# Kernel optimization log

Hardware: AMD Instinct MI355X
Metric: run time of the kernel (lower is better)

Reference implementation:

```python
import jax, jax.numpy as jnp
import numpy as np

N = 30000
E = 300000
F_IN = 512
OUT = 1024


def _l2norm(x):
    # F.normalize(x, p=2, dim=1) with eps=1e-12
    n = jnp.linalg.norm(x, axis=1, keepdims=True)
    return x / jnp.maximum(n, 1e-12)


def _gcn_conv(x, W, b, row, col, w):
    # PyG GCNConv: x' = D^-1/2 (A + I) D^-1/2 (x W) + b, self-loops weight 1
    n = x.shape[0]
    h = x @ W  # [n, out]
    deg = jax.ops.segment_sum(w, row, num_segments=n)
    dinv = jnp.where(deg > 0, jax.lax.rsqrt(deg), 0.0)
    nw = dinv[row] * w * dinv[col]  # per-edge norm
    agg = jax.ops.segment_sum(h[col] * nw[:, None], row, num_segments=n)
    return agg + b


def _forward(x, edge_index, edge_weight, beta,
             W1, b1, W2, b2, W3, b3, Wmu, bmu, Wlv, blv, Wd1, bd1, Wd2, bd2):
    n = x.shape[0]
    loops = jnp.arange(n, dtype=edge_index.dtype)
    row = jnp.concatenate([edge_index[0], loops])
    col = jnp.concatenate([edge_index[1], loops])
    w = jnp.concatenate([edge_weight, jnp.ones((n,), edge_weight.dtype)])

    out1 = jax.nn.relu(_l2norm(_gcn_conv(x, W1, b1, row, col, w)))
    out2 = jax.nn.relu(_l2norm(_gcn_conv(out1, W2, b2, row, col, w)))
    out3 = jax.nn.relu(_l2norm(_gcn_conv(out2, W3, b3, row, col, w)))

    mu = out3 @ Wmu + bmu
    logvar = out3 @ Wlv + blv

    # reparameterize(mu, beta * logvar) with eps ~ N(0,1)*0.01
    lv = beta * logvar
    std = jnp.exp(0.5 * lv)
    eps = jax.random.normal(jax.random.key(42), std.shape, std.dtype) * 0.01
    z = mu + eps * std

    # batch=None pooling: global max + mean over nodes
    pooled = jnp.concatenate([jnp.max(z, axis=0), jnp.mean(z, axis=0)])[None, :]  # [1, 1024]

    h = jax.nn.relu(pooled @ Wd1 + bd1)
    recon_x = jax.nn.sigmoid(h @ Wd2 + bd2)
    return recon_x, mu, logvar


def setup_inputs() -> dict:
    key = jax.random.key(0)
    ks = jax.random.split(key, 20)
    def glorot(k, shape):
        lim = np.sqrt(6.0 / (shape[0] + shape[1]))
        return jax.random.uniform(k, shape, jnp.float32, -lim, lim)
    H = 512
    return {
        "x": jax.random.normal(ks[0], (N, F_IN), jnp.float32),
        "edge_index": jax.random.randint(ks[1], (2, E), 0, N, jnp.int64),
        "edge_weight": jax.random.uniform(ks[2], (E,), jnp.float32),
        "beta": 1,
        "W1": glorot(ks[3], (F_IN, 1024)), "b1": jnp.zeros((1024,), jnp.float32),
        "W2": glorot(ks[4], (1024, 512)), "b2": jnp.zeros((512,), jnp.float32),
        "W3": glorot(ks[5], (512, 256)), "b3": jnp.zeros((256,), jnp.float32),
        "Wmu": glorot(ks[6], (256, H)), "bmu": jnp.zeros((H,), jnp.float32),
        "Wlv": glorot(ks[7], (256, H)), "blv": jnp.zeros((H,), jnp.float32),
        "Wd1": glorot(ks[8], (2 * H, 2 * H)), "bd1": jnp.zeros((2 * H,), jnp.float32),
        "Wd2": glorot(ks[9], (2 * H, OUT)), "bd2": jnp.zeros((OUT,), jnp.float32),
    }


def reference(x, edge_index, edge_weight, beta,
              W1, b1, W2, b2, W3, b3, Wmu, bmu, Wlv, blv, Wd1, bd1, Wd2, bd2):
    return _forward(x, edge_index, edge_weight, beta,
                    W1, b1, W2, b2, W3, b3, Wmu, bmu, Wlv, blv, Wd1, bd1, Wd2, bd2)
```

## Files before the change

kernel.cpp:

```cpp
#include <hip/hip_runtime.h>
#include <cstdint>
#include <cstddef>

#define NNODE      30000
#define FIN        512
#define H1DIM      1024
#define H2DIM      512
#define H3DIM      256
#define HDIM       512
#define HALF_ROWS  15000
#define HALF_ELEMS 7680000u
#define PP_ROWS    16
#define PP_BLOCKS  938
#define PM_BLOCKS  64
#define NPANEL     118
#define NSCAN      118

typedef __attribute__((ext_vector_type(8))) short s16x8;
typedef __attribute__((ext_vector_type(4))) short s16x4;
typedef __attribute__((ext_vector_type(4))) float f32x4;

__device__ __forceinline__ short f2bf(float f) {
    uint32_t u = __float_as_uint(f);
    uint32_t r = (u + 0x7FFFu + ((u >> 16) & 1u)) >> 16;
    return (short)r;
}
__device__ __forceinline__ float bf2f(short s) {
    return __uint_as_float(((uint32_t)(uint16_t)s) << 16);
}

__device__ __forceinline__ void threefry2x32(uint32_t k0, uint32_t k1,
                                             uint32_t& x0, uint32_t& x1) {
    uint32_t ks0 = k0, ks1 = k1, ks2 = k0 ^ k1 ^ 0x1BD11BDAu;
    const uint32_t R0[4] = {13u, 15u, 26u, 6u};
    const uint32_t R1[4] = {17u, 29u, 16u, 24u};
    x0 += ks0; x1 += ks1;
#pragma unroll
    for (int g = 0; g < 5; ++g) {
        const uint32_t* R = (g & 1) ? R1 : R0;
#pragma unroll
        for (int r = 0; r < 4; ++r) {
            x0 += x1;
            x1 = (x1 << R[r]) | (x1 >> (32u - R[r]));
            x1 ^= x0;
        }
        uint32_t ks_a = (g % 3 == 0) ? ks1 : (g % 3 == 1 ? ks2 : ks0);
        uint32_t ks_b = (g % 3 == 0) ? ks2 : (g % 3 == 1 ? ks0 : ks1);
        x0 += ks_a;
        x1 += ks_b + (uint32_t)(g + 1);
    }
}

__device__ __forceinline__ float jax_normal(uint32_t bits) {
    uint32_t fb = (bits >> 9) | 0x3F800000u;
    float f = __uint_as_float(fb) - 1.0f;
    const float lo = -0.99999994f;
    float u = fmaf(f, 2.0f, lo);
    u = fmaxf(u, lo);
    return 1.41421356237f * erfinvf(u);
}

__global__ void deg_cnt_kernel(const int* __restrict__ row, const float* __restrict__ w,
                               float* __restrict__ deg, int* __restrict__ cnt, int E) {
    int e = blockIdx.x * 256 + threadIdx.x;
    if (e < E) {
        int r = row[e];
        atomicAdd(&deg[r], w[e]);
        atomicAdd(&cnt[r], 1);
    }
}

__global__ void dinv_kernel(const float* __restrict__ deg, float* __restrict__ dinv, int n) {
    int i = blockIdx.x * 256 + threadIdx.x;
    if (i < n) dinv[i] = rsqrtf(deg[i] + 1.0f);
}

__global__ void rsqrt_clamp_kernel(float* __restrict__ ss, int n) {
    int i = blockIdx.x * 256 + threadIdx.x;
    if (i < n) ss[i] = 1.0f / fmaxf(sqrtf(ss[i]), 1e-12f);
}

__global__ __launch_bounds__(256) void rp_blocksum(const int* __restrict__ cnt,
                                                   int* __restrict__ bsum) {
    __shared__ int sh[256];
    int i = blockIdx.x * 256 + threadIdx.x;
    sh[threadIdx.x] = (i < NNODE) ? cnt[i] : 0;
    __syncthreads();
    for (int o = 128; o; o >>= 1) {
        if (threadIdx.x < o) sh[threadIdx.x] += sh[threadIdx.x + o];
        __syncthreads();
    }
    if (threadIdx.x == 0) bsum[blockIdx.x] = sh[0];
}

__global__ __launch_bounds__(128) void rp_scan(int* __restrict__ bsum, int nb) {
    __shared__ int sh[128];
    int t = threadIdx.x;
    sh[t] = (t < nb) ? bsum[t] : 0;
    __syncthreads();
    for (int o = 1; o < 128; o <<= 1) {
        int v = (t >= o) ? sh[t - o] : 0;
        __syncthreads();
        sh[t] += v;
        __syncthreads();
    }
    if (t < nb) bsum[t] = (t == 0) ? 0 : sh[t - 1];
}

__global__ __launch_bounds__(256) void rp_write(const int* __restrict__ cnt,
                                                const int* __restrict__ bsum,
                                                int* __restrict__ rowptr, int E) {
    __shared__ int sh[256];
    int i = blockIdx.x * 256 + threadIdx.x;
    int v = (i < NNODE) ? cnt[i] : 0;
    sh[threadIdx.x] = v;
    __syncthreads();
    for (int o = 1; o < 256; o <<= 1) {
        int x = (threadIdx.x >= o) ? sh[threadIdx.x - o] : 0;
        __syncthreads();
        sh[threadIdx.x] += x;
        __syncthreads();
    }
    if (i < NNODE) rowptr[i] = bsum[blockIdx.x] + sh[threadIdx.x] - v;
    if (i == NNODE - 1) rowptr[NNODE] = E;
}

__global__ void scatter_edges(const int* __restrict__ row, const int* __restrict__ col,
                              const float* __restrict__ w, const float* __restrict__ dinv,
                              const int* __restrict__ rowptr, int* __restrict__ fill,
                              int* __restrict__ ecol, float* __restrict__ eval, int E) {
    int e = blockIdx.x * 256 + threadIdx.x;
    if (e < E) {
        int r = row[e], c = col[e];
        int pos = rowptr[r] + atomicAdd(&fill[r], 1);
        ecol[pos] = c;
        eval[pos] = dinv[r] * w[e] * dinv[c];
    }
}

__global__ void f32_to_bf16(const float* __restrict__ in, short* __restrict__ out, int n4) {
    int i = blockIdx.x * 256 + threadIdx.x;
    if (i < n4) {
        float4 v = ((const float4*)in)[i];
        s16x4 s = { f2bf(v.x), f2bf(v.y), f2bf(v.z), f2bf(v.w) };
        *(s16x4*)(out + (size_t)i * 4) = s;
    }
}

__global__ __launch_bounds__(256) void transpose_bf16(const float* __restrict__ W,
                                                      short* __restrict__ Wt, int K, int N) {
    __shared__ float t[32][33];
    int kb = blockIdx.y * 32, nb = blockIdx.x * 32;
    int tx = threadIdx.x & 31, ty = threadIdx.x >> 5;
#pragma unroll
    for (int i = 0; i < 32; i += 8)
        if (kb + ty + i < K && nb + tx < N)
            t[ty + i][tx] = W[(size_t)(kb + ty + i) * N + nb + tx];
    __syncthreads();
#pragma unroll
    for (int i = 0; i < 32; i += 8)
        if (nb + ty + i < N && kb + tx < K)
            Wt[(size_t)(nb + ty + i) * K + kb + tx] = f2bf(t[tx][ty + i]);
}

template <int F, bool FUSE>
__global__ __launch_bounds__(256) void spmm_bf16(const int* __restrict__ rowptr,
                                                 const int* __restrict__ ecol,
                                                 const float* __restrict__ eval,
                                                 const float* __restrict__ dinv,
                                                 const short* __restrict__ h,
                                                 const float* __restrict__ bias,
                                                 short* __restrict__ out) {
    constexpr int NE = F / 64;
    int lane = threadIdx.x & 63;
    int r = blockIdx.x * 4 + (threadIdx.x >> 6);
    if (r >= NNODE) return;
    float d = dinv[r];
    float dd = d * d;
    float acc[NE];
    {
        const short* p = h + (size_t)r * F + lane * NE;
        if constexpr (NE == 8) {
            s16x8 v = *(const s16x8*)p;
#pragma unroll
            for (int j = 0; j < 8; ++j) acc[j] = dd * bf2f(v[j]);
        } else {
            s16x4 v = *(const s16x4*)p;
#pragma unroll
            for (int j = 0; j < 4; ++j) acc[j] = dd * bf2f(v[j]);
        }
    }
    int e0 = rowptr[r], e1 = rowptr[r + 1];
    int e = e0;
    for (; e + 2 <= e1; e += 2) {
        int c0 = ecol[e], c1 = ecol[e + 1];
        float w0 = eval[e], w1 = eval[e + 1];
        const short* p0 = h + (size_t)c0 * F + lane * NE;
        const short* p1 = h + (size_t)c1 * F + lane * NE;
        if constexpr (NE == 8) {
            s16x8 v0 = *(const s16x8*)p0;
            s16x8 v1 = *(const s16x8*)p1;
#pragma unroll
            for (int j = 0; j < 8; ++j) acc[j] = fmaf(w0, bf2f(v0[j]), acc[j]);
#pragma unroll
            for (int j = 0; j < 8; ++j) acc[j] = fmaf(w1, bf2f(v1[j]), acc[j]);
        } else {
            s16x4 v0 = *(const s16x4*)p0;
            s16x4 v1 = *(const s16x4*)p1;
#pragma unroll
            for (int j = 0; j < 4; ++j) acc[j] = fmaf(w0, bf2f(v0[j]), acc[j]);
#pragma unroll
            for (int j = 0; j < 4; ++j) acc[j] = fmaf(w1, bf2f(v1[j]), acc[j]);
        }
    }
    if (e < e1) {
        int c = ecol[e];
        float nw = eval[e];
        const short* p = h + (size_t)c * F + lane * NE;
        if constexpr (NE == 8) {
            s16x8 v = *(const s16x8*)p;
#pragma unroll
            for (int j = 0; j < 8; ++j) acc[j] = fmaf(nw, bf2f(v[j]), acc[j]);
        } else {
            s16x4 v = *(const s16x4*)p;
#pragma unroll
            for (int j = 0; j < 4; ++j) acc[j] = fmaf(nw, bf2f(v[j]), acc[j]);
        }
    }
    short* o = out + (size_t)r * F + lane * NE;
    if (FUSE) {
        const float* bp = bias + lane * NE;
        float ss = 0.f;
#pragma unroll
        for (int j = 0; j < NE; ++j) { acc[j] += bp[j]; ss += acc[j] * acc[j]; }
#pragma unroll
        for (int off = 32; off; off >>= 1) ss += __shfl_xor(ss, off);
        float rinv = 1.0f / fmaxf(sqrtf(ss), 1e-12f);
#pragma unroll
        for (int j = 0; j < NE; ++j) acc[j] = fmaxf(acc[j] * rinv, 0.f);
    }
    if constexpr (NE == 8) {
        s16x8 s;
#pragma unroll
        for (int j = 0; j < 8; ++j) s[j] = f2bf(acc[j]);
        *(s16x8*)o = s;
    } else {
        s16x4 s;
#pragma unroll
        for (int j = 0; j < 4; ++j) s[j] = f2bf(acc[j]);
        *(s16x4*)o = s;
    }
}

#define STAGE_TILE(buf_, kt_)                                                              \
  {                                                                                        \
    const int k0_ = (kt_) << 6;                                                            \
    _Pragma("unroll")                                                                      \
    for (int i_ = 0; i_ < 4; ++i_) {                                                       \
      int c_ = i_ * 8 + w;                                                                 \
      int tr_ = c_ * 8 + srow;                                                             \
      __builtin_amdgcn_global_load_lds(                                                    \
          (const __attribute__((address_space(1))) void*)(A + (size_t)(m0 + tr_) * K + k0_ + scol), \
          (__attribute__((address_space(3))) void*)(&sA[buf_][c_ * 512]), 16, 0, 0);       \
    }                                                                                      \
    _Pragma("unroll")                                                                      \
    for (int i_ = 0; i_ < 4; ++i_) {                                                       \
      int c_ = i_ * 8 + w;                                                                 \
      int tr_ = c_ * 8 + srow;                                                             \
      __builtin_amdgcn_global_load_lds(                                                    \
          (const __attribute__((address_space(1))) void*)(Bt + (size_t)(n0 + tr_) * K + k0_ + scol), \
          (__attribute__((address_space(3))) void*)(&sB[buf_][c_ * 512]), 16, 0, 0);       \
    }                                                                                      \
  }

template <typename OutT, bool ADD_BIAS, int EPI>
__global__ __launch_bounds__(512) void gemm_bf16(const short* __restrict__ A,
                                                 const short* __restrict__ Bt,
                                                 const float* __restrict__ bias,
                                                 const float* __restrict__ bias2,
                                                 OutT* __restrict__ C,
                                                 float* __restrict__ C2,
                                                 float* __restrict__ ssbuf,
                                                 int M, int N, int K) {
    __shared__ short sA[2][256 * 64];
    __shared__ short sB[2][256 * 64];
    const int tid = threadIdx.x;
    const int lane = tid & 63;
    const int w = tid >> 6;
    const int wm = w >> 2, wn = w & 3;

    const int nwg = gridDim.x;
    const int orig = blockIdx.x;
    const int q = nwg >> 3, rr = nwg & 7;
    const int xcd = orig & 7;
    const int base = (xcd < rr) ? xcd * (q + 1) : rr * (q + 1) + (xcd - rr) * q;
    const int wgid = base + (orig >> 3);
    const int nx = N >> 8;
    const int lg = __builtin_ctz(nx);
    const int pid = wgid >> lg;
    const int cblk = wgid & (nx - 1);
    const int m0 = pid << 8;
    const int n0 = cblk << 8;

    const int srow = lane >> 3;
    const int scol = ((lane & 7) ^ srow) * 8;

    f32x4 acc[8][4] = {};

    const int lrow = lane & 15;
    const int jhi = lane >> 4;

    const int nkt = K >> 6;
    int cur = 0;
    STAGE_TILE(0, 0);
    __syncthreads();

    for (int kt = 0; kt < nkt; ++kt) {
        if (kt + 1 < nkt) STAGE_TILE(cur ^ 1, kt + 1);

        s16x8 bfr[4][2];
#pragma unroll
        for (int fn = 0; fn < 4; ++fn) {
            int lr = wn * 64 + fn * 16 + lrow;
            const short* bptr = &sB[cur][lr * 64];
            int sl0 = jhi ^ (lr & 7);
            bfr[fn][0] = *(const s16x8*)&bptr[sl0 << 3];
            bfr[fn][1] = *(const s16x8*)&bptr[(sl0 ^ 4) << 3];
        }
        __builtin_amdgcn_s_setprio(1);
#pragma unroll
        for (int fm = 0; fm < 8; ++fm) {
            int lr = wm * 128 + fm * 16 + lrow;
            const short* aptr = &sA[cur][lr * 64];
            int sl0 = jhi ^ (lr & 7);
            s16x8 a0 = *(const s16x8*)&aptr[sl0 << 3];
            s16x8 a1 = *(const s16x8*)&aptr[(sl0 ^ 4) << 3];
#pragma unroll
            for (int fn = 0; fn < 4; ++fn) {
                acc[fm][fn] = __builtin_amdgcn_mfma_f32_16x16x32_bf16(a0, bfr[fn][0], acc[fm][fn], 0, 0, 0);
                acc[fm][fn] = __builtin_amdgcn_mfma_f32_16x16x32_bf16(a1, bfr[fn][1], acc[fm][fn], 0, 0, 0);
            }
        }
        __builtin_amdgcn_s_setprio(0);
        __syncthreads();
        cur ^= 1;
    }

    const int crow = (lane >> 4) * 4;
    const int ccol = lane & 15;

    if constexpr (EPI == 1) {
        float ssl[8][4] = {};
#pragma unroll
        for (int fm = 0; fm < 8; ++fm) {
#pragma unroll
            for (int fn = 0; fn < 4; ++fn) {
                int n = n0 + wn * 64 + fn * 16 + ccol;
                float b = bias[n];
#pragma unroll
                for (int r = 0; r < 4; ++r) {
                    float o = acc[fm][fn][r] + b;
                    ssl[fm][r] += o * o;
                    int m = m0 + wm * 128 + fm * 16 + crow + r;
                    if (m < M) C[(size_t)m * N + n] = (OutT)f2bf(fmaxf(o, 0.f));
                }
            }
        }
#pragma unroll
        for (int fm = 0; fm < 8; ++fm)
#pragma unroll
            for (int r = 0; r < 4; ++r) {
                float v = ssl[fm][r];
                v += __shfl_xor(v, 1); v += __shfl_xor(v, 2);
                v += __shfl_xor(v, 4); v += __shfl_xor(v, 8);
                int m = m0 + wm * 128 + fm * 16 + crow + r;
                if (ccol == 0 && m < M) atomicAdd(&ssbuf[m], v);
            }
    } else if constexpr (EPI == 2) {
#pragma unroll
        for (int fm = 0; fm < 8; ++fm) {
#pragma unroll
            for (int fn = 0; fn < 4; ++fn) {
                int n = n0 + wn * 64 + fn * 16 + ccol;
#pragma unroll
                for (int r = 0; r < 4; ++r) {
                    int m = m0 + wm * 128 + fm * 16 + crow + r;
                    if (m < M) {
                        float sc = ssbuf[m];
                        C[(size_t)m * N + n] = (OutT)f2bf(acc[fm][fn][r] * sc);
                    }
                }
            }
        }
    } else if constexpr (EPI == 3) {
        const int half = N >> 1;
#pragma unroll
        for (int fm = 0; fm < 8; ++fm) {
#pragma unroll
            for (int fn = 0; fn < 4; ++fn) {
                int n = n0 + wn * 64 + fn * 16 + ccol;
                bool hi = n >= half;
                float b = hi ? bias2[n - half] : bias[n];
                float* Cp = hi ? C2 : (float*)C;
                int nc = hi ? (n - half) : n;
#pragma unroll
                for (int r = 0; r < 4; ++r) {
                    int m = m0 + wm * 128 + fm * 16 + crow + r;
                    if (m < M) Cp[(size_t)m * half + nc] = acc[fm][fn][r] + b;
                }
            }
        }
    } else {
#pragma unroll
        for (int fm = 0; fm < 8; ++fm) {
#pragma unroll
            for (int fn = 0; fn < 4; ++fn) {
                int n = n0 + wn * 64 + fn * 16 + ccol;
                float b = ADD_BIAS ? bias[n] : 0.f;
#pragma unroll
                for (int r = 0; r < 4; ++r) {
                    int m = m0 + wm * 128 + fm * 16 + crow + r;
                    if (m < M) {
                        float o = acc[fm][fn][r] + b;
                        if constexpr (sizeof(OutT) == 2) C[(size_t)m * N + n] = (OutT)f2bf(o);
                        else                             C[(size_t)m * N + n] = o;
                    }
                }
            }
        }
    }
}

__global__ __launch_bounds__(256) void pool_partial(const float* __restrict__ mu,
                                                    const float* __restrict__ lv,
                                                    const uint32_t* __restrict__ beta_p,
                                                    float* __restrict__ pmax,
                                                    float* __restrict__ psum) {
    uint32_t bb = beta_p[0];
    float beta = (bb & 0x7F800000u) ? __uint_as_float(bb) : (float)(int)bb;
    int b = blockIdx.x;
    int r0 = b * PP_ROWS;
    int r1 = min(r0 + PP_ROWS, HALF_ROWS);
    int c = threadIdx.x * 2;
    float m0 = -INFINITY, m1 = -INFINITY, s0 = 0.f, s1 = 0.f;
    for (int r = r0; r < r1; ++r) {
        size_t ia = (size_t)r * HDIM + c;
        size_t ib = (size_t)(r + HALF_ROWS) * HDIM + c;
        float2 mua = *(const float2*)&mu[ia];
        float2 lva = *(const float2*)&lv[ia];
        float2 mub = *(const float2*)&mu[ib];
        float2 lvb = *(const float2*)&lv[ib];
        uint32_t idx0 = (uint32_t)r * 512u + (uint32_t)c;
        uint32_t xa0 = idx0,     ya0 = idx0 + HALF_ELEMS;
        uint32_t xa1 = idx0 + 1, ya1 = idx0 + 1 + HALF_ELEMS;
        threefry2x32(0u, 42u, xa0, ya0);
        threefry2x32(0u, 42u, xa1, ya1);
        float za0 = mua.x + 0.01f * jax_normal(xa0) * __expf(0.5f * beta * lva.x);
        float zb0 = mub.x + 0.01f * jax_normal(ya0) * __expf(0.5f * beta * lvb.x);
        float za1 = mua.y + 0.01f * jax_normal(xa1) * __expf(0.5f * beta * lva.y);
        float zb1 = mub.y + 0.01f * jax_normal(ya1) * __expf(0.5f * beta * lvb.y);
        m0 = fmaxf(m0, fmaxf(za0, zb0)); s0 += za0 + zb0;
        m1 = fmaxf(m1, fmaxf(za1, zb1)); s1 += za1 + zb1;
    }
    pmax[(size_t)b * HDIM + c]     = m0;
    pmax[(size_t)b * HDIM + c + 1] = m1;
    psum[(size_t)b * HDIM + c]     = s0;
    psum[(size_t)b * HDIM + c + 1] = s1;
}

__global__ __launch_bounds__(256) void pool_mid(const float* __restrict__ pmax,
                                                const float* __restrict__ psum,
                                                float* __restrict__ pmax2,
                                                float* __restrict__ psum2) {
    int g = blockIdx.x;
    int b0 = g * 15;
    int b1 = min(b0 + 15, PP_BLOCKS);
#pragma unroll
    for (int pass = 0; pass < 2; ++pass) {
        int c = threadIdx.x + pass * 256;
        float m = -INFINITY, s = 0.f;
        for (int b = b0; b < b1; ++b) {
            m = fmaxf(m, pmax[(size_t)b * HDIM + c]);
            s += psum[(size_t)b * HDIM + c];
        }
        pmax2[(size_t)g * HDIM + c] = m;
        psum2[(size_t)g * HDIM + c] = s;
    }
}

__global__ void pool_final(const float* __restrict__ pmax2, const float* __restrict__ psum2,
                           float* __restrict__ pooled) {
    int c = blockIdx.x * 256 + threadIdx.x;
    if (c < HDIM) {
        float m = -INFINITY, s = 0.f;
#pragma unroll
        for (int b = 0; b < PM_BLOCKS; ++b) {
            m = fmaxf(m, pmax2[(size_t)b * HDIM + c]);
            s += psum2[(size_t)b * HDIM + c];
        }
        pooled[c] = m;
        pooled[HDIM + c] = s / 30000.0f;
    }
}

__global__ __launch_bounds__(256) void dense_partial(const float* __restrict__ in,
                                                     const float* __restrict__ W,
                                                     float* __restrict__ part) {
    int by = blockIdx.y;
    int j = blockIdx.x * 256 + threadIdx.x;
    __shared__ float sin_[128];
    if (threadIdx.x < 128) sin_[threadIdx.x] = in[by * 128 + threadIdx.x];
    __syncthreads();
    float acc = 0.f;
#pragma unroll 8
    for (int i = 0; i < 128; ++i)
        acc = fmaf(sin_[i], W[(size_t)(by * 128 + i) * 1024 + j], acc);
    part[(size_t)by * 1024 + j] = acc;
}

__global__ void dense_final(const float* __restrict__ part, const float* __restrict__ bias,
                            float* __restrict__ out, int act) {
    int j = blockIdx.x * 256 + threadIdx.x;
    float acc = bias[j];
#pragma unroll
    for (int s = 0; s < 8; ++s) acc += part[(size_t)s * 1024 + j];
    out[j] = act ? (1.0f / (1.0f + __expf(-acc))) : fmaxf(acc, 0.f);
}

extern "C" void kernel_launch(void* const* d_in, const int* in_sizes, int n_in,
                              void* d_out, int out_size, void* d_ws, size_t ws_size,
                              hipStream_t stream) {
    const float* x   = (const float*)d_in[0];
    const int*   ei  = (const int*)d_in[1];
    const float* ew  = (const float*)d_in[2];
    const uint32_t* beta = (const uint32_t*)d_in[3];
    const float* W1  = (const float*)d_in[4];
    const float* b1  = (const float*)d_in[5];
    const float* W2  = (const float*)d_in[6];
    const float* b2  = (const float*)d_in[7];
    const float* W3  = (const float*)d_in[8];
    const float* b3  = (const float*)d_in[9];
    const float* Wmu = (const float*)d_in[10];
    const float* bmu = (const float*)d_in[11];
    const float* Wlv = (const float*)d_in[12];
    const float* blv = (const float*)d_in[13];
    const float* Wd1 = (const float*)d_in[14];
    const float* bd1 = (const float*)d_in[15];
    const float* Wd2 = (const float*)d_in[16];
    const float* bd2 = (const float*)d_in[17];

    const int E = in_sizes[2];
    const int M = NNODE;

    float* out    = (float*)d_out;
    float* mu_out = out + 1024;
    float* lv_out = out + 1024 + (size_t)M * HDIM;

    char* Wp = (char*)d_ws;
    short* slotA  = (short*)(Wp);
    short* slotB  = (short*)(Wp + 61603840);
    short* xb     = (short*)(Wp + 123207680);
    short* W1t    = (short*)(Wp + 154009600);
    short* W2t    = (short*)(Wp + 155058176);
    short* W3t    = (short*)(Wp + 156106752);
    short* Wmut   = (short*)(Wp + 156368896);
    short* Wlvt   = (short*)(Wp + 156631040);
    float* deg    = (float*)(Wp + 156893184);
    float* dinv   = (float*)(Wp + 157013184);
    int*   cnt    = (int*)  (Wp + 157133184);
    int*   fill   = (int*)  (Wp + 157253184);
    float* ssbuf  = (float*)(Wp + 157373184);
    int*   rowptr = (int*)  (Wp + 157493184);
    int*   ecol   = (int*)  (Wp + 157613188);
    float* eval   = (float*)(Wp + 158813188);
    float* pmax   = (float*)(Wp + 160013188);
    float* psum   = (float*)(Wp + 161934212);
    float* pmax2  = (float*)(Wp + 163855236);
    float* psum2  = (float*)(Wp + 163986308);
    float* pooled = (float*)(Wp + 164117380);
    float* hdec   = (float*)(Wp + 164121476);
    float* dpart  = (float*)(Wp + 164125572);
    int*   bsum   = (int*)pmax;

    const int* row = ei;
    const int* col = ei + E;

    hipMemsetAsync(deg, 0, 600000, stream);

    deg_cnt_kernel<<<(E + 255) / 256, 256, 0, stream>>>(row, ew, deg, cnt, E);
    dinv_kernel<<<(M + 255) / 256, 256, 0, stream>>>(deg, dinv, M);
    rp_blocksum<<<NSCAN, 256, 0, stream>>>(cnt, bsum);
    rp_scan<<<1, 128, 0, stream>>>(bsum, NSCAN);
    rp_write<<<NSCAN, 256, 0, stream>>>(cnt, bsum, rowptr, E);
    scatter_edges<<<(E + 255) / 256, 256, 0, stream>>>(row, col, ew, dinv, rowptr, fill,
                                                       ecol, eval, E);

    f32_to_bf16<<<(M * FIN / 4 + 255) / 256, 256, 0, stream>>>(x, xb, M * FIN / 4);
    {
        dim3 b(256);
        transpose_bf16<<<dim3(H1DIM / 32, FIN / 32),   b, 0, stream>>>(W1,  W1t,  FIN,   H1DIM);
        transpose_bf16<<<dim3(H2DIM / 32, H1DIM / 32), b, 0, stream>>>(W2,  W2t,  H1DIM, H2DIM);
        transpose_bf16<<<dim3(H3DIM / 32, H2DIM / 32), b, 0, stream>>>(W3,  W3t,  H2DIM, H3DIM);
        transpose_bf16<<<dim3(HDIM / 32,  H3DIM / 32), b, 0, stream>>>(Wmu, Wmut, H3DIM, HDIM);
        transpose_bf16<<<dim3(HDIM / 32,  H3DIM / 32), b, 0, stream>>>(Wlv, Wlvt, H3DIM, HDIM);
    }

    const int SPMM_GRID = (M + 3) / 4;

    spmm_bf16<512, false><<<SPMM_GRID, 256, 0, stream>>>(rowptr, ecol, eval, dinv, xb,
                                                         nullptr, slotA);
    gemm_bf16<short, true, 1><<<(H1DIM / 256) * NPANEL, 512, 0, stream>>>(
        slotA, W1t, b1, nullptr, slotB, nullptr, ssbuf, M, H1DIM, FIN);
    rsqrt_clamp_kernel<<<(M + 255) / 256, 256, 0, stream>>>(ssbuf, M);

    gemm_bf16<short, false, 2><<<(H2DIM / 256) * NPANEL, 512, 0, stream>>>(
        slotB, W2t, nullptr, nullptr, slotA, nullptr, ssbuf, M, H2DIM, H1DIM);
    spmm_bf16<512, true><<<SPMM_GRID, 256, 0, stream>>>(rowptr, ecol, eval, dinv, slotA,
                                                        b2, slotB);

    gemm_bf16<short, false, 0><<<(H3DIM / 256) * NPANEL, 512, 0, stream>>>(
        slotB, W3t, nullptr, nullptr, slotA, nullptr, nullptr, M, H3DIM, H2DIM);
    spmm_bf16<256, true><<<SPMM_GRID, 256, 0, stream>>>(rowptr, ecol, eval, dinv, slotA,
                                                        b3, slotB);

    gemm_bf16<float, true, 3><<<((2 * HDIM) / 256) * NPANEL, 512, 0, stream>>>(
        slotB, Wmut, bmu, blv, mu_out, lv_out, nullptr, M, 2 * HDIM, H3DIM);

    pool_partial<<<PP_BLOCKS, 256, 0, stream>>>(mu_out, lv_out, beta, pmax, psum);
    pool_mid<<<PM_BLOCKS, 256, 0, stream>>>(pmax, psum, pmax2, psum2);
    pool_final<<<2, 256, 0, stream>>>(pmax2, psum2, pooled);

    dense_partial<<<dim3(4, 8), 256, 0, stream>>>(pooled, Wd1, dpart);
    dense_final<<<4, 256, 0, stream>>>(dpart, bd1, hdec, 0);
    dense_partial<<<dim3(4, 8), 256, 0, stream>>>(hdec, Wd2, dpart);
    dense_final<<<4, 256, 0, stream>>>(dpart, bd2, out, 1);
}
```

Baseline: 492.1 us.

## Fold norm rsqrt into GEMM epilogue, unroll SpMM edges by four, finer pooling

Removes the standalone rsqrt_clamp kernel and computes the inverse L2 norm inside the EPI==2 GEMM epilogue, once per row instead of once per element load. The SpMM edge loop is unrolled from two to four neighbours to put more gathers in flight. Pool partial blocks are halved in rows and doubled in count, with the workspace offsets and the mid-level reduction resized to match. Each wave now repeats the sqrt/divide and carries more registers in the SpMM loop.

```diff
diff --git a/kernel.cpp b/kernel.cpp
--- a/kernel.cpp
+++ b/kernel.cpp
@@ -10,9 +10,9 @@
 #define HDIM       512
 #define HALF_ROWS  15000
 #define HALF_ELEMS 7680000u
-#define PP_ROWS    16
-#define PP_BLOCKS  938
-#define PM_BLOCKS  64
+#define PP_ROWS    8
+#define PP_BLOCKS  1875
+#define PM_BLOCKS  63
 #define NPANEL     118
 #define NSCAN      118
 
@@ -73,11 +73,6 @@
 __global__ void dinv_kernel(const float* __restrict__ deg, float* __restrict__ dinv, int n) {
     int i = blockIdx.x * 256 + threadIdx.x;
     if (i < n) dinv[i] = rsqrtf(deg[i] + 1.0f);
-}
-
-__global__ void rsqrt_clamp_kernel(float* __restrict__ ss, int n) {
-    int i = blockIdx.x * 256 + threadIdx.x;
-    if (i < n) ss[i] = 1.0f / fmaxf(sqrtf(ss[i]), 1e-12f);
 }
 
 __global__ __launch_bounds__(256) void rp_blocksum(const int* __restrict__ cnt,
@@ -192,28 +187,42 @@
     }
     int e0 = rowptr[r], e1 = rowptr[r + 1];
     int e = e0;
-    for (; e + 2 <= e1; e += 2) {
-        int c0 = ecol[e], c1 = ecol[e + 1];
-        float w0 = eval[e], w1 = eval[e + 1];
+    for (; e + 4 <= e1; e += 4) {
+        int   c0 = ecol[e],     c1 = ecol[e + 1], c2 = ecol[e + 2], c3 = ecol[e + 3];
+        float w0 = eval[e],     w1 = eval[e + 1], w2 = eval[e + 2], w3 = eval[e + 3];
         const short* p0 = h + (size_t)c0 * F + lane * NE;
         const short* p1 = h + (size_t)c1 * F + lane * NE;
+        const short* p2 = h + (size_t)c2 * F + lane * NE;
+        const short* p3 = h + (size_t)c3 * F + lane * NE;
         if constexpr (NE == 8) {
             s16x8 v0 = *(const s16x8*)p0;
             s16x8 v1 = *(const s16x8*)p1;
+            s16x8 v2 = *(const s16x8*)p2;
+            s16x8 v3 = *(const s16x8*)p3;
 #pragma unroll
             for (int j = 0; j < 8; ++j) acc[j] = fmaf(w0, bf2f(v0[j]), acc[j]);
 #pragma unroll
             for (int j = 0; j < 8; ++j) acc[j] = fmaf(w1, bf2f(v1[j]), acc[j]);
+#pragma unroll
+            for (int j = 0; j < 8; ++j) acc[j] = fmaf(w2, bf2f(v2[j]), acc[j]);
+#pragma unroll
+            for (int j = 0; j < 8; ++j) acc[j] = fmaf(w3, bf2f(v3[j]), acc[j]);
         } else {
             s16x4 v0 = *(const s16x4*)p0;
             s16x4 v1 = *(const s16x4*)p1;
+            s16x4 v2 = *(const s16x4*)p2;
+            s16x4 v3 = *(const s16x4*)p3;
 #pragma unroll
             for (int j = 0; j < 4; ++j) acc[j] = fmaf(w0, bf2f(v0[j]), acc[j]);
 #pragma unroll
             for (int j = 0; j < 4; ++j) acc[j] = fmaf(w1, bf2f(v1[j]), acc[j]);
-        }
-    }
-    if (e < e1) {
+#pragma unroll
+            for (int j = 0; j < 4; ++j) acc[j] = fmaf(w2, bf2f(v2[j]), acc[j]);
+#pragma unroll
+            for (int j = 0; j < 4; ++j) acc[j] = fmaf(w3, bf2f(v3[j]), acc[j]);
+        }
+    }
+    for (; e < e1; ++e) {
         int c = ecol[e];
         float nw = eval[e];
         const short* p = h + (size_t)c * F + lane * NE;
@@ -380,15 +389,14 @@
 #pragma unroll
         for (int fm = 0; fm < 8; ++fm) {
 #pragma unroll
-            for (int fn = 0; fn < 4; ++fn) {
-                int n = n0 + wn * 64 + fn * 16 + ccol;
-#pragma unroll
-                for (int r = 0; r < 4; ++r) {
-                    int m = m0 + wm * 128 + fm * 16 + crow + r;
-                    if (m < M) {
-                        float sc = ssbuf[m];
-                        C[(size_t)m * N + n] = (OutT)f2bf(acc[fm][fn][r] * sc);
-                    }
+            for (int r = 0; r < 4; ++r) {
+                int m = m0 + wm * 128 + fm * 16 + crow + r;
+                if (m >= M) continue;
+                float sc = 1.0f / fmaxf(sqrtf(ssbuf[m]), 1e-12f);
+#pragma unroll
+                for (int fn = 0; fn < 4; ++fn) {
+                    int n = n0 + wn * 64 + fn * 16 + ccol;
+                    C[(size_t)m * N + n] = (OutT)f2bf(acc[fm][fn][r] * sc);
                 }
             }
         }
@@ -473,8 +481,8 @@
                                                 float* __restrict__ pmax2,
                                                 float* __restrict__ psum2) {
     int g = blockIdx.x;
-    int b0 = g * 15;
-    int b1 = min(b0 + 15, PP_BLOCKS);
+    int b0 = g * 30;
+    int b1 = min(b0 + 30, PP_BLOCKS);
 #pragma unroll
     for (int pass = 0; pass < 2; ++pass) {
         int c = threadIdx.x + pass * 256;
@@ -574,12 +582,12 @@
     int*   ecol   = (int*)  (Wp + 157613188);
     float* eval   = (float*)(Wp + 158813188);
     float* pmax   = (float*)(Wp + 160013188);
-    float* psum   = (float*)(Wp + 161934212);
-    float* pmax2  = (float*)(Wp + 163855236);
-    float* psum2  = (float*)(Wp + 163986308);
-    float* pooled = (float*)(Wp + 164117380);
-    float* hdec   = (float*)(Wp + 164121476);
-    float* dpart  = (float*)(Wp + 164125572);
+    float* psum   = (float*)(Wp + 163853188);
+    float* pmax2  = (float*)(Wp + 167693188);
+    float* psum2  = (float*)(Wp + 167822212);
+    float* pooled = (float*)(Wp + 167951236);
+    float* hdec   = (float*)(Wp + 167955332);
+    float* dpart  = (float*)(Wp + 167959428);
     int*   bsum   = (int*)pmax;
 
     const int* row = ei;
@@ -611,7 +619,6 @@
                                                          nullptr, slotA);
     gemm_bf16<short, true, 1><<<(H1DIM / 256) * NPANEL, 512, 0, stream>>>(
         slotA, W1t, b1, nullptr, slotB, nullptr, ssbuf, M, H1DIM, FIN);
-    rsqrt_clamp_kernel<<<(M + 255) / 256, 256, 0, stream>>>(ssbuf, M);
 
     gemm_bf16<short, false, 2><<<(H2DIM / 256) * NPANEL, 512, 0, stream>>>(
         slotB, W2t, nullptr, nullptr, slotA, nullptr, ssbuf, M, H2DIM, H1DIM);
```

Result: no change. 483.2 us (-1.8%).
